# Performance work log

Hardware: AMD Instinct MI355X
Metric: run time of the kernel (lower is better)

Reference implementation:

```python
import jax, jax.numpy as jnp
import numpy as np

N_NODES, N_EDGES, N_FEAT, N_GRAPHS = 100_000, 1_600_000, 3, 512
FENG = jnp.array([4, 8, 9, 12, 13, 14])  # feng_filters(): second-order pairs with scale2 > scale1
LEAKY_SLOPE = 0.01


def _wavelet_constructor():
    # Psi_j = P^{2^{j-1}} - P^{2^j}, j = 1..4, over 17 diffusion levels P^0..P^16
    W = np.zeros((4, 17), dtype=np.float32)
    for j, (a, b) in enumerate([(1, 2), (2, 4), (4, 8), (8, 16)]):
        W[j, a] = 1.0
        W[j, b] = -1.0
    return jnp.asarray(W)


def _gcn_edges(edge_index, n):
    # gcn_norm with self-loops: w_ij = d_i^-1/2 d_j^-1/2 on A + I
    loop = jnp.arange(n)
    src = jnp.concatenate([edge_index[0], loop])
    dst = jnp.concatenate([edge_index[1], loop])
    deg = jax.ops.segment_sum(jnp.ones_like(dst, dtype=jnp.float32), dst, num_segments=n)
    dinv = jnp.where(deg > 0, jax.lax.rsqrt(deg), 0.0)
    w = dinv[src] * dinv[dst]
    return src, dst, w


def _diffuse(x, src, dst, w, n):
    # lazy random walk: 0.5 * (x + P_norm x), x: [N, C, k]
    agg = jax.ops.segment_sum(w[:, None, None] * x[src], dst, num_segments=n)
    return 0.5 * (x + agg)


def _scatter_features(x, edge_index):
    n, c = x.shape
    src, dst, w = _gcn_edges(edge_index, n)
    Wav = _wavelet_constructor()

    s0 = x[:, :, None]                                   # [N, C, 1]
    levels = [s0]
    for _ in range(16):
        levels.append(_diffuse(levels[-1], src, dst, w, n))
    D = jnp.stack(levels)                                # [17, N, C, 1]
    sub = jnp.einsum('wt,tnck->wnck', Wav, D)[..., 0]    # [4, N, C]
    s1 = jnp.abs(jnp.transpose(sub, (1, 2, 0)))          # [N, C, 4]

    levels2 = [s1]
    for _ in range(16):
        levels2.append(_diffuse(levels2[-1], src, dst, w, n))
    D2 = jnp.stack(levels2)                              # [17, N, C, 4]
    sub2 = jnp.einsum('wt,tncf->wncf', Wav, D2)          # [4, N, C, 4]
    # reproduce the exact torch transpose/reshape sequence of LEGS Scatter
    t = jnp.abs(jnp.transpose(sub2, (1, 0, 2, 3)).reshape(n, c, 16))  # [N, C, 16]
    s2 = jnp.swapaxes(t, 1, 2)[:, FENG]                  # [N, 6, C]

    xcat = jnp.concatenate([s0, s1], axis=2)             # [N, C, 5]
    xcat = jnp.swapaxes(xcat, 1, 2)                      # [N, 5, C]
    xcat = jnp.concatenate([xcat, s2], axis=1)           # [N, 11, C]
    return xcat.reshape(n, 11 * c)                       # [N, 33]


def _scatter_moments(x, batch, num_graphs):
    # per-graph mean / variance / skew (3 central moments), concatenated -> [G, 3*F]
    cnt = jax.ops.segment_sum(jnp.ones((x.shape[0],), x.dtype), batch, num_segments=num_graphs)
    cnt = jnp.maximum(cnt, 1.0)[:, None]
    mean = jax.ops.segment_sum(x, batch, num_segments=num_graphs) / cnt
    dev = x - mean[batch]
    var = jax.ops.segment_sum(dev * dev, batch, num_segments=num_graphs) / cnt
    skew = jax.ops.segment_sum(dev * dev * dev, batch, num_segments=num_graphs) / cnt
    return jnp.concatenate([mean, var, skew], axis=1)


def setup_inputs() -> dict:
    key = jax.random.key(0)
    ks = jax.random.split(key, 8)
    x = jax.random.normal(ks[0], (N_NODES, N_FEAT), dtype=jnp.float32)
    edge_index = jax.random.randint(ks[1], (2, N_EDGES), 0, N_NODES)
    batch = jnp.sort(jax.random.randint(ks[2], (N_NODES,), 0, N_GRAPHS))

    def lin(k, fan_in, fan_out):
        k1, k2 = jax.random.split(k)
        bound = 1.0 / np.sqrt(fan_in)
        W = jax.random.uniform(k1, (fan_in, fan_out), minval=-bound, maxval=bound, dtype=jnp.float32)
        b = jax.random.uniform(k2, (fan_out,), minval=-bound, maxval=bound, dtype=jnp.float32)
        return W, b

    W1, b1 = lin(ks[3], 99, 128)
    W2, b2 = lin(ks[4], 128, 64)
    W3, b3 = lin(ks[5], 64, 64)
    We, be = lin(ks[6], 64, 32)
    Wc, bc = lin(ks[7], 32, 1)
    return {"x": x, "W1": W1, "b1": b1, "W2": W2, "b2": b2, "W3": W3, "b3": b3,
            "We": We, "be": be, "Wc": Wc, "bc": bc,
            "edge_index": edge_index, "batch": batch, "num_graphs": N_GRAPHS}


def reference(x, W1, b1, W2, b2, W3, b3, We, be, Wc, bc, edge_index, batch, num_graphs):
    act = lambda v: jax.nn.leaky_relu(v, LEAKY_SLOPE)
    feats = _scatter_features(x, edge_index)              # [N, 33]
    h = _scatter_moments(feats, batch, num_graphs)        # [G, 99]
    h = act(h)
    h = act(h @ W1 + b1)        # dropout is identity (p=0.0)
    h = act(h @ W2 + b2)
    h = h @ W3 + b3             # no activation before embedding layer (as in source)
    embedding = h @ We + be
    output = embedding @ Wc + bc  # classifier applied to embedding (pre-activation)
    return embedding, output
```

## Files before the change

kernel.cpp:

```cpp
#include <hip/hip_runtime.h>

#define N_NODES 100000
#define N_EDGES 1600000
#define NG      512
#define NSB     98
#define SUBR    1024
#define SCAP    20480
#define SD      96
#define B2BLK   256
#define B2E     ((N_EDGES + B2BLK - 1) / B2BLK)
#define PCAP    18432

static __device__ __forceinline__ float lrelu(float v) {
    return v >= 0.0f ? v : 0.01f * v;
}

__global__ void k_zero_i32(int* __restrict__ p, int n) {
    int i = blockIdx.x * blockDim.x + threadIdx.x;
    if (i < n) p[i] = 0;
}

__global__ void k_dinv(const int* __restrict__ counts, float* __restrict__ dinv,
                       float* __restrict__ dinv2, float* __restrict__ sdeg) {
    int i = blockIdx.x * blockDim.x + threadIdx.x;
    if (i < N_NODES) {
        float deg = (float)(counts[i] + 1);
        float s = sqrtf(deg);
        sdeg[i] = s;
        dinv[i] = 1.0f / s;
        dinv2[i] = 1.0f / deg;
    }
}

__global__ __launch_bounds__(256) void k_bin2(const int* __restrict__ esrc,
                                              const int* __restrict__ edst,
                                              int* __restrict__ gcur,
                                              uint2* __restrict__ gbuf) {
    __shared__ uint2 st[NSB][SD];
    __shared__ int lcnt[NSB];
    __shared__ int gbase[NSB];
    for (int i = threadIdx.x; i < NSB; i += 256) lcnt[i] = 0;
    __syncthreads();
    int base = blockIdx.x * B2E;
    int end = base + B2E; if (end > N_EDGES) end = N_EDGES;
    for (int e = base + (int)threadIdx.x; e < end; e += 256) {
        int d = edst[e];
        int s = esrc[e];
        int b = d >> 10;
        int pos = atomicAdd(&lcnt[b], 1);
        if (pos < SD) {
            st[b][pos] = make_uint2((unsigned)s, (unsigned)d);
        } else {
            int g = atomicAdd(&gcur[b], 1);
            gbuf[(size_t)b * SCAP + g] = make_uint2((unsigned)s, (unsigned)d);
        }
    }
    __syncthreads();
    if (threadIdx.x < NSB) {
        int c = lcnt[threadIdx.x]; if (c > SD) c = SD;
        gbase[threadIdx.x] = atomicAdd(&gcur[threadIdx.x], c);
    }
    __syncthreads();
    for (int b = 0; b < NSB; ++b) {
        int cnt = lcnt[b]; if (cnt > SD) cnt = SD;
        int gb = gbase[b];
        for (int i = threadIdx.x; i < cnt; i += 256)
            gbuf[(size_t)b * SCAP + gb + i] = st[b][i];
    }
}

__global__ __launch_bounds__(256) void k_count_s(const int* __restrict__ gcur,
                                                 const uint2* __restrict__ gbuf,
                                                 int* __restrict__ counts) {
    __shared__ int h[SUBR];
    int sb = blockIdx.x;
    int lo = sb * SUBR;
    int nr = N_NODES - lo; if (nr > SUBR) nr = SUBR;
    for (int i = threadIdx.x; i < nr; i += 256) h[i] = 0;
    __syncthreads();
    int n = gcur[sb];
    const uint2* bb = gbuf + (size_t)sb * SCAP;
    for (int i = threadIdx.x; i < n; i += 256)
        atomicAdd(&h[(int)bb[i].y - lo], 1);
    __syncthreads();
    for (int i = threadIdx.x; i < nr; i += 256)
        counts[lo + i] = h[i];
}

__global__ void k_scan_block(const int* __restrict__ counts, int* __restrict__ offsets,
                             int* __restrict__ bsums, int n) {
    __shared__ int tmp[1024];
    int gid = blockIdx.x * 1024 + threadIdx.x;
    int v = (gid < n) ? counts[gid] : 0;
    tmp[threadIdx.x] = v;
    __syncthreads();
    for (int off = 1; off < 1024; off <<= 1) {
        int t = (threadIdx.x >= off) ? tmp[threadIdx.x - off] : 0;
        __syncthreads();
        tmp[threadIdx.x] += t;
        __syncthreads();
    }
    if (gid < n) offsets[gid + 1] = tmp[threadIdx.x];
    if (threadIdx.x == 1023) bsums[blockIdx.x] = tmp[1023];
}

__global__ void k_scan_bsums(int* __restrict__ bsums, int nb) {
    if (blockIdx.x == 0 && threadIdx.x == 0) {
        int acc = 0;
        for (int b = 0; b < nb; ++b) { int v = bsums[b]; bsums[b] = acc; acc += v; }
    }
}

__global__ void k_scan_add(int* __restrict__ offsets, const int* __restrict__ bsums, int n) {
    int gid = blockIdx.x * 1024 + threadIdx.x;
    if (gid < n) offsets[gid + 1] += bsums[blockIdx.x];
    if (gid == 0) offsets[0] = 0;
}

__global__ __launch_bounds__(256) void k_place(const int* __restrict__ gcur,
                                               const uint2* __restrict__ gbuf,
                                               const int* __restrict__ offsets,
                                               int* __restrict__ csr_src) {
    __shared__ int cur[SUBR];
    __shared__ int stage[PCAP];
    int sb = blockIdx.x;
    int lo = sb * SUBR;
    int nr = N_NODES - lo; if (nr > SUBR) nr = SUBR;
    int base = offsets[lo];
    int total = offsets[lo + nr] - base;
    for (int i = threadIdx.x; i < nr; i += 256)
        cur[i] = offsets[lo + i] - base;
    __syncthreads();
    int n = gcur[sb];
    const uint2* bb = gbuf + (size_t)sb * SCAP;
    for (int i = threadIdx.x; i < n; i += 256) {
        uint2 e = bb[i];
        int p = atomicAdd(&cur[(int)e.y - lo], 1);
        if (p < PCAP) stage[p] = (int)e.x;
        else csr_src[base + p] = (int)e.x;
    }
    __syncthreads();
    int wtot = total < PCAP ? total : PCAP;
    for (int i = threadIdx.x; i < wtot; i += 256)
        csr_src[base + i] = stage[i];
}

__global__ void k_vinit(const float* __restrict__ x, const float* __restrict__ dinv,
                        float4* __restrict__ v) {
    int i = blockIdx.x * blockDim.x + threadIdx.x;
    if (i >= N_NODES) return;
    float di = dinv[i];
    v[i] = make_float4(di * x[i * 3 + 0], di * x[i * 3 + 1], di * x[i * 3 + 2], 0.0f);
}

__global__ __launch_bounds__(256) void k_vdiff3(
    const float4* __restrict__ xin, float4* __restrict__ xout,
    const int* __restrict__ offs, const int* __restrict__ csrc,
    const float* __restrict__ dinv2) {
    int t = blockIdx.x * 256 + threadIdx.x;
    if (t >= N_NODES * 8) return;
    int h = t & 7;
    int i = t >> 3;
    int b = offs[i], e = offs[i + 1];
    float a0 = 0.0f, a1 = 0.0f, a2 = 0.0f;
    int p = b + h;
    while (p < e) {
        int idx[4];
        int c = 0;
#pragma unroll
        for (int j = 0; j < 4; ++j) {
            int pp = p + j * 8;
            if (pp < e) { idx[j] = csrc[pp]; c = j + 1; }
        }
#pragma unroll
        for (int j = 0; j < 4; ++j) {
            if (j < c) {
                float4 xv = xin[idx[j]];
                a0 += xv.x; a1 += xv.y; a2 += xv.z;
            }
        }
        p += 32;
    }
    a0 += __shfl_xor(a0, 1, 64); a1 += __shfl_xor(a1, 1, 64); a2 += __shfl_xor(a2, 1, 64);
    a0 += __shfl_xor(a0, 2, 64); a1 += __shfl_xor(a1, 2, 64); a2 += __shfl_xor(a2, 2, 64);
    a0 += __shfl_xor(a0, 4, 64); a1 += __shfl_xor(a1, 4, 64); a2 += __shfl_xor(a2, 4, 64);
    if (h == 0) {
        float d2 = dinv2[i];
        float4 sv = xin[i];
        xout[i] = make_float4(0.5f * (sv.x + d2 * (a0 + sv.x)),
                              0.5f * (sv.y + d2 * (a1 + sv.y)),
                              0.5f * (sv.z + d2 * (a2 + sv.z)), 0.0f);
    }
}

__global__ __launch_bounds__(256) void k_vdiff12(
    const float4* __restrict__ xin, float4* __restrict__ xout,
    const int* __restrict__ offs, const int* __restrict__ csrc,
    const float* __restrict__ dinv2) {
    int t = blockIdx.x * 256 + threadIdx.x;
    if (t >= N_NODES * 8) return;
    int h = t & 7;
    int i = t >> 3;
    int b = offs[i], e = offs[i + 1];
    float a[12];
#pragma unroll
    for (int c = 0; c < 12; ++c) a[c] = 0.0f;
    int p = b + h;
    while (p < e) {
        int idx[4];
        int c = 0;
#pragma unroll
        for (int j = 0; j < 4; ++j) {
            int pp = p + j * 8;
            if (pp < e) { idx[j] = csrc[pp]; c = j + 1; }
        }
#pragma unroll
        for (int j = 0; j < 4; ++j) {
            if (j < c) {
                int s = idx[j];
                float4 b0 = xin[s * 4 + 0];
                float4 b1 = xin[s * 4 + 1];
                float4 b2 = xin[s * 4 + 2];
                a[0] += b0.x; a[1] += b0.y; a[2]  += b0.z; a[3]  += b0.w;
                a[4] += b1.x; a[5] += b1.y; a[6]  += b1.z; a[7]  += b1.w;
                a[8] += b2.x; a[9] += b2.y; a[10] += b2.z; a[11] += b2.w;
            }
        }
        p += 32;
    }
#pragma unroll
    for (int c = 0; c < 12; ++c) {
        a[c] += __shfl_xor(a[c], 1, 64);
        a[c] += __shfl_xor(a[c], 2, 64);
        a[c] += __shfl_xor(a[c], 4, 64);
    }
    if (h == 0) {
        float d2 = dinv2[i];
        float4 s0 = xin[i * 4 + 0], s1 = xin[i * 4 + 1], s2 = xin[i * 4 + 2];
        xout[i * 4 + 0] = make_float4(0.5f * (s0.x + d2 * (a[0] + s0.x)),
                                      0.5f * (s0.y + d2 * (a[1] + s0.y)),
                                      0.5f * (s0.z + d2 * (a[2] + s0.z)),
                                      0.5f * (s0.w + d2 * (a[3] + s0.w)));
        xout[i * 4 + 1] = make_float4(0.5f * (s1.x + d2 * (a[4] + s1.x)),
                                      0.5f * (s1.y + d2 * (a[5] + s1.y)),
                                      0.5f * (s1.z + d2 * (a[6] + s1.z)),
                                      0.5f * (s1.w + d2 * (a[7] + s1.w)));
        xout[i * 4 + 2] = make_float4(0.5f * (s2.x + d2 * (a[8] + s2.x)),
                                      0.5f * (s2.y + d2 * (a[9] + s2.y)),
                                      0.5f * (s2.z + d2 * (a[10] + s2.z)),
                                      0.5f * (s2.w + d2 * (a[11] + s2.w)));
    }
}

__global__ void k_s1v(const float4* __restrict__ L1, const float4* __restrict__ L2,
                      const float4* __restrict__ L4, const float4* __restrict__ L8,
                      const float4* __restrict__ L16, float* __restrict__ s1vp) {
    int i = blockIdx.x * blockDim.x + threadIdx.x;
    if (i >= N_NODES) return;
    float4 v[5];
    v[0] = L1[i]; v[1] = L2[i]; v[2] = L4[i]; v[3] = L8[i]; v[4] = L16[i];
    float* out = s1vp + (size_t)i * 16;
#pragma unroll
    for (int f = 0; f < 4; ++f) {
        out[0 * 4 + f] = fabsf(v[f].x - v[f + 1].x);
        out[1 * 4 + f] = fabsf(v[f].y - v[f + 1].y);
        out[2 * 4 + f] = fabsf(v[f].z - v[f + 1].z);
    }
}

__global__ void k_feats(const float* __restrict__ x, const float* __restrict__ s1vp,
                        const float* __restrict__ M1, const float* __restrict__ M2,
                        const float* __restrict__ M4, const float* __restrict__ M8,
                        const float* __restrict__ M16, const float* __restrict__ sdeg,
                        float* __restrict__ feats) {
    int i = blockIdx.x * blockDim.x + threadIdx.x;
    if (i >= N_NODES) return;
    float sd = sdeg[i];
    float* out = feats + (size_t)i * 33;
    out[0] = x[i * 3 + 0];
    out[1] = x[i * 3 + 1];
    out[2] = x[i * 3 + 2];
    for (int r = 1; r <= 4; ++r)
        for (int c = 0; c < 3; ++c)
            out[r * 3 + c] = sd * s1vp[(size_t)i * 16 + c * 4 + (r - 1)];
    const float* Ms[5] = {M1, M2, M4, M8, M16};
    const int FENG[6] = {4, 8, 9, 12, 13, 14};
    for (int m = 0; m < 6; ++m) {
        for (int c2 = 0; c2 < 3; ++c2) {
            int idx = c2 * 16 + FENG[m];
            int w = idx / 12, rem = idx % 12, cc = rem / 4, f = rem % 4;
            float v = Ms[w][(size_t)i * 16 + cc * 4 + f] - Ms[w + 1][(size_t)i * 16 + cc * 4 + f];
            out[(5 + m) * 3 + c2] = fabsf(sd * v);
        }
    }
}

static __device__ __forceinline__ int lower_bound_i(const int* __restrict__ a, int n, int key) {
    int lo = 0, hi = n;
    while (lo < hi) { int mid = (lo + hi) >> 1; if (a[mid] < key) lo = mid + 1; else hi = mid; }
    return lo;
}

__global__ __launch_bounds__(256) void k_moments(
    const float* __restrict__ feats, const int* __restrict__ batch,
    float* __restrict__ h0) {
    __shared__ float P1[4][33], P2[4][33], P3[4][33];
    int g = blockIdx.x;
    int lo = lower_bound_i(batch, N_NODES, g);
    int hi = lower_bound_i(batch, N_NODES, g + 1);
    int w = threadIdx.x >> 6;
    int l = threadIdx.x & 63;
    float s1 = 0.0f, s2 = 0.0f, s3 = 0.0f;
    if (l < 33) {
        for (int i = lo + w; i < hi; i += 4) {
            float v = feats[(size_t)i * 33 + l];
            s1 += v;
            s2 += v * v;
            s3 += v * v * v;
        }
        P1[w][l] = s1; P2[w][l] = s2; P3[w][l] = s3;
    }
    __syncthreads();
    if (threadIdx.x < 33) {
        int c = threadIdx.x;
        float S1 = P1[0][c] + P1[1][c] + P1[2][c] + P1[3][c];
        float S2 = P2[0][c] + P2[1][c] + P2[2][c] + P2[3][c];
        float S3 = P3[0][c] + P3[1][c] + P3[2][c] + P3[3][c];
        float cnt = (float)((hi - lo) > 1 ? (hi - lo) : 1);
        float mu  = S1 / cnt;
        float ex2 = S2 / cnt;
        float ex3 = S3 / cnt;
        float var = ex2 - mu * mu;
        float skw = ex3 - 3.0f * mu * ex2 + 2.0f * mu * mu * mu;
        h0[g * 99 + c]      = lrelu(mu);
        h0[g * 99 + 33 + c] = lrelu(var);
        h0[g * 99 + 66 + c] = lrelu(skw);
    }
}

__global__ __launch_bounds__(128) void k_mlp(
    const float* __restrict__ h0,
    const float* __restrict__ W1, const float* __restrict__ b1,
    const float* __restrict__ W2, const float* __restrict__ b2,
    const float* __restrict__ W3, const float* __restrict__ b3,
    const float* __restrict__ We, const float* __restrict__ be,
    const float* __restrict__ Wc, const float* __restrict__ bc,
    float* __restrict__ emb, float* __restrict__ outp) {
    __shared__ float s0[99], s1[128], s2[64], s3[64], s4[32];
    int g = blockIdx.x;
    int t = threadIdx.x;
    if (t < 99) s0[t] = h0[g * 99 + t];
    __syncthreads();
    {
        float a = b1[t];
        for (int k = 0; k < 99; ++k) a += s0[k] * W1[k * 128 + t];
        s1[t] = lrelu(a);
    }
    __syncthreads();
    if (t < 64) {
        float a = b2[t];
        for (int k = 0; k < 128; ++k) a += s1[k] * W2[k * 64 + t];
        s2[t] = lrelu(a);
    }
    __syncthreads();
    if (t < 64) {
        float a = b3[t];
        for (int k = 0; k < 64; ++k) a += s2[k] * W3[k * 64 + t];
        s3[t] = a;
    }
    __syncthreads();
    if (t < 32) {
        float a = be[t];
        for (int k = 0; k < 64; ++k) a += s3[k] * We[k * 32 + t];
        s4[t] = a;
        emb[g * 32 + t] = a;
    }
    __syncthreads();
    if (t == 0) {
        float a = bc[0];
        for (int k = 0; k < 32; ++k) a += s4[k] * Wc[k];
        outp[g] = a;
    }
}

extern "C" void kernel_launch(void* const* d_in, const int* in_sizes, int n_in,
                              void* d_out, int out_size, void* d_ws, size_t ws_size,
                              hipStream_t stream) {
    const float* x   = (const float*)d_in[0];
    const float* W1  = (const float*)d_in[1];
    const float* b1  = (const float*)d_in[2];
    const float* W2  = (const float*)d_in[3];
    const float* b2  = (const float*)d_in[4];
    const float* W3  = (const float*)d_in[5];
    const float* b3  = (const float*)d_in[6];
    const float* We  = (const float*)d_in[7];
    const float* be  = (const float*)d_in[8];
    const float* Wc  = (const float*)d_in[9];
    const float* bc  = (const float*)d_in[10];
    const int*   eix = (const int*)d_in[11];
    const int*   batch = (const int*)d_in[12];
    const int* esrc = eix;
    const int* edst = eix + N_EDGES;

    char* ws = (char*)d_ws;
    size_t off = 0;
    auto alloc = [&](size_t bytes) -> void* {
        void* p = ws + off;
        off = (off + bytes + 255) & ~(size_t)255;
        return p;
    };
    int*   counts  = (int*)alloc((size_t)N_NODES * 4);
    int*   offsets = (int*)alloc((size_t)(N_NODES + 1) * 4);
    float* dinv    = (float*)alloc((size_t)N_NODES * 4);
    float* dinv2   = (float*)alloc((size_t)N_NODES * 4);
    float* sdeg    = (float*)alloc((size_t)N_NODES * 4);
    int*   bsums   = (int*)alloc(1024 * 4);
    int*   gcur    = (int*)alloc(NSB * 4);
    uint2* gbuf    = (uint2*)alloc((size_t)NSB * SCAP * 8);
    int*   csr_src = (int*)alloc((size_t)N_EDGES * 4);
    float4* v0     = (float4*)alloc((size_t)N_NODES * 16);
    float4* p1[7];
    for (int i = 0; i < 7; ++i) p1[i] = (float4*)alloc((size_t)N_NODES * 16);
    float* s1vp = (float*)alloc((size_t)N_NODES * 16 * 4);
    float* p2[7];
    for (int i = 0; i < 7; ++i) p2[i] = (float*)alloc((size_t)N_NODES * 16 * 4);
    float* feats = (float*)alloc((size_t)N_NODES * 33 * 4);
    float* h0 = (float*)alloc((size_t)NG * 99 * 4);
    (void)ws_size; (void)in_sizes; (void)n_in; (void)out_size;

    const int TB = 256;
    const int gbN = (N_NODES + TB - 1) / TB;
    const int nbScan = (N_NODES + 1023) / 1024;

    hipLaunchKernelGGL(k_zero_i32, dim3(1), dim3(TB), 0, stream, gcur, NSB);
    hipLaunchKernelGGL(k_bin2, dim3(B2BLK), dim3(TB), 0, stream, esrc, edst, gcur, gbuf);
    hipLaunchKernelGGL(k_count_s, dim3(NSB), dim3(TB), 0, stream, gcur, gbuf, counts);
    hipLaunchKernelGGL(k_dinv, dim3(gbN), dim3(TB), 0, stream, counts, dinv, dinv2, sdeg);
    hipLaunchKernelGGL(k_scan_block, dim3(nbScan), dim3(1024), 0, stream, counts, offsets, bsums, N_NODES);
    hipLaunchKernelGGL(k_scan_bsums, dim3(1), dim3(1), 0, stream, bsums, nbScan);
    hipLaunchKernelGGL(k_scan_add, dim3(nbScan), dim3(1024), 0, stream, offsets, bsums, N_NODES);
    hipLaunchKernelGGL(k_place, dim3(NSB), dim3(TB), 0, stream, gcur, gbuf, offsets, csr_src);

    hipLaunchKernelGGL(k_vinit, dim3(gbN), dim3(TB), 0, stream, x, dinv, v0);

    const int saveT[5] = {1, 2, 4, 8, 16};

    const float4* prev = v0;
    float4* saves1[5];
    {
        int si = 0, sc = 0;
        const int gb = (N_NODES * 8 + TB - 1) / TB;
        for (int t = 1; t <= 16; ++t) {
            float4* outb;
            if (si < 5 && t == saveT[si]) { outb = p1[si]; saves1[si] = outb; ++si; }
            else { outb = p1[5 + sc]; sc ^= 1; }
            hipLaunchKernelGGL(k_vdiff3, dim3(gb), dim3(TB), 0, stream,
                               prev, outb, offsets, csr_src, dinv2);
            prev = outb;
        }
    }
    hipLaunchKernelGGL(k_s1v, dim3(gbN), dim3(TB), 0, stream,
                       saves1[0], saves1[1], saves1[2], saves1[3], saves1[4], s1vp);

    float* saves2[5];
    {
        const float* prev2 = s1vp;
        int si = 0, sc = 0;
        const int gb = (N_NODES * 8 + TB - 1) / TB;
        for (int t = 1; t <= 16; ++t) {
            float* outb;
            if (si < 5 && t == saveT[si]) { outb = p2[si]; saves2[si] = outb; ++si; }
            else { outb = p2[5 + sc]; sc ^= 1; }
            hipLaunchKernelGGL(k_vdiff12, dim3(gb), dim3(TB), 0, stream,
                               (const float4*)prev2, (float4*)outb, offsets, csr_src, dinv2);
            prev2 = outb;
        }
    }

    hipLaunchKernelGGL(k_feats, dim3(gbN), dim3(TB), 0, stream,
                       x, s1vp, saves2[0], saves2[1], saves2[2], saves2[3], saves2[4], sdeg, feats);
    hipLaunchKernelGGL(k_moments, dim3(NG), dim3(256), 0, stream, feats, batch, h0);

    float* emb  = (float*)d_out;
    float* outp = (float*)d_out + NG * 32;
    hipLaunchKernelGGL(k_mlp, dim3(NG), dim3(128), 0, stream,
                       h0, W1, b1, W2, b2, W3, b3, We, be, Wc, bc, emb, outp);
}
```

Baseline: 716.6 us.

## Fuse preprocessing, epilogues and head kernels to cut launch count

Merges the degree-inverse and vinit kernels, replaces the three-kernel global scan with a per-superblock scan inside k_place plus a tiny superblock-base scan, and folds the s1 wavelet computation and feature assembly into the last diffusion step of each stage via a LAST template. The moments and MLP kernels become one head kernel. The aim is to drop about seven launches and the round trips through intermediate buffers such as the level-16 outputs and h0. In exchange, the last diffusion kernels run heavier epilogues on one thread per node, which adds register pressure.

```diff
diff --git a/kernel.cpp b/kernel.cpp
--- a/kernel.cpp
+++ b/kernel.cpp
@@ -20,15 +20,17 @@
     if (i < n) p[i] = 0;
 }
 
-__global__ void k_dinv(const int* __restrict__ counts, float* __restrict__ dinv,
-                       float* __restrict__ dinv2, float* __restrict__ sdeg) {
+__global__ void k_dinv_vinit(const int* __restrict__ counts, const float* __restrict__ x,
+                             float* __restrict__ dinv2, float* __restrict__ sdeg,
+                             float4* __restrict__ v0) {
     int i = blockIdx.x * blockDim.x + threadIdx.x;
     if (i < N_NODES) {
         float deg = (float)(counts[i] + 1);
         float s = sqrtf(deg);
         sdeg[i] = s;
-        dinv[i] = 1.0f / s;
         dinv2[i] = 1.0f / deg;
+        float di = 1.0f / s;
+        v0[i] = make_float4(di * x[i * 3 + 0], di * x[i * 3 + 1], di * x[i * 3 + 2], 0.0f);
     }
 }
 
@@ -87,76 +89,77 @@
         counts[lo + i] = h[i];
 }
 
-__global__ void k_scan_block(const int* __restrict__ counts, int* __restrict__ offsets,
-                             int* __restrict__ bsums, int n) {
-    __shared__ int tmp[1024];
-    int gid = blockIdx.x * 1024 + threadIdx.x;
-    int v = (gid < n) ? counts[gid] : 0;
-    tmp[threadIdx.x] = v;
-    __syncthreads();
-    for (int off = 1; off < 1024; off <<= 1) {
-        int t = (threadIdx.x >= off) ? tmp[threadIdx.x - off] : 0;
-        __syncthreads();
-        tmp[threadIdx.x] += t;
-        __syncthreads();
-    }
-    if (gid < n) offsets[gid + 1] = tmp[threadIdx.x];
-    if (threadIdx.x == 1023) bsums[blockIdx.x] = tmp[1023];
-}
-
-__global__ void k_scan_bsums(int* __restrict__ bsums, int nb) {
+__global__ void k_sbscan(const int* __restrict__ gcur, int* __restrict__ sbbase) {
     if (blockIdx.x == 0 && threadIdx.x == 0) {
         int acc = 0;
-        for (int b = 0; b < nb; ++b) { int v = bsums[b]; bsums[b] = acc; acc += v; }
-    }
-}
-
-__global__ void k_scan_add(int* __restrict__ offsets, const int* __restrict__ bsums, int n) {
-    int gid = blockIdx.x * 1024 + threadIdx.x;
-    if (gid < n) offsets[gid + 1] += bsums[blockIdx.x];
-    if (gid == 0) offsets[0] = 0;
+        for (int b = 0; b < NSB; ++b) { sbbase[b] = acc; acc += gcur[b]; }
+    }
 }
 
 __global__ __launch_bounds__(256) void k_place(const int* __restrict__ gcur,
                                                const uint2* __restrict__ gbuf,
-                                               const int* __restrict__ offsets,
+                                               const int* __restrict__ sbbase,
+                                               const int* __restrict__ counts,
+                                               int* __restrict__ offsets,
                                                int* __restrict__ csr_src) {
     __shared__ int cur[SUBR];
+    __shared__ int wsum[256];
     __shared__ int stage[PCAP];
     int sb = blockIdx.x;
     int lo = sb * SUBR;
     int nr = N_NODES - lo; if (nr > SUBR) nr = SUBR;
-    int base = offsets[lo];
-    int total = offsets[lo + nr] - base;
-    for (int i = threadIdx.x; i < nr; i += 256)
-        cur[i] = offsets[lo + i] - base;
+    int t = threadIdx.x;
+    int c0[4];
+    int b4 = t * 4;
+    int s = 0;
+#pragma unroll
+    for (int j = 0; j < 4; ++j) {
+        int ii = b4 + j;
+        c0[j] = (ii < nr) ? counts[lo + ii] : 0;
+        s += c0[j];
+    }
+    wsum[t] = s;
+    __syncthreads();
+    for (int off = 1; off < 256; off <<= 1) {
+        int v = (t >= off) ? wsum[t - off] : 0;
+        __syncthreads();
+        wsum[t] += v;
+        __syncthreads();
+    }
+    int run = (t == 0) ? 0 : wsum[t - 1];
+#pragma unroll
+    for (int j = 0; j < 4; ++j) {
+        int ii = b4 + j;
+        if (ii < SUBR) cur[ii] = run;
+        run += c0[j];
+    }
+    __syncthreads();
+    int gb = sbbase[sb];
+    for (int i = t; i < nr; i += 256) offsets[lo + i] = gb + cur[i];
+    if (sb == NSB - 1 && t == 0) offsets[N_NODES] = N_EDGES;
     __syncthreads();
     int n = gcur[sb];
     const uint2* bb = gbuf + (size_t)sb * SCAP;
-    for (int i = threadIdx.x; i < n; i += 256) {
+    for (int i = t; i < n; i += 256) {
         uint2 e = bb[i];
         int p = atomicAdd(&cur[(int)e.y - lo], 1);
         if (p < PCAP) stage[p] = (int)e.x;
-        else csr_src[base + p] = (int)e.x;
-    }
-    __syncthreads();
-    int wtot = total < PCAP ? total : PCAP;
-    for (int i = threadIdx.x; i < wtot; i += 256)
-        csr_src[base + i] = stage[i];
-}
-
-__global__ void k_vinit(const float* __restrict__ x, const float* __restrict__ dinv,
-                        float4* __restrict__ v) {
-    int i = blockIdx.x * blockDim.x + threadIdx.x;
-    if (i >= N_NODES) return;
-    float di = dinv[i];
-    v[i] = make_float4(di * x[i * 3 + 0], di * x[i * 3 + 1], di * x[i * 3 + 2], 0.0f);
-}
-
+        else csr_src[gb + p] = (int)e.x;
+    }
+    __syncthreads();
+    int wtot = n < PCAP ? n : PCAP;
+    for (int i = t; i < wtot; i += 256)
+        csr_src[gb + i] = stage[i];
+}
+
+template <bool LAST>
 __global__ __launch_bounds__(256) void k_vdiff3(
     const float4* __restrict__ xin, float4* __restrict__ xout,
     const int* __restrict__ offs, const int* __restrict__ csrc,
-    const float* __restrict__ dinv2) {
+    const float* __restrict__ dinv2,
+    const float4* __restrict__ L1, const float4* __restrict__ L2,
+    const float4* __restrict__ L4, const float4* __restrict__ L8,
+    float* __restrict__ s1vp) {
     int t = blockIdx.x * 256 + threadIdx.x;
     if (t >= N_NODES * 8) return;
     int h = t & 7;
@@ -187,16 +190,39 @@
     if (h == 0) {
         float d2 = dinv2[i];
         float4 sv = xin[i];
-        xout[i] = make_float4(0.5f * (sv.x + d2 * (a0 + sv.x)),
-                              0.5f * (sv.y + d2 * (a1 + sv.y)),
-                              0.5f * (sv.z + d2 * (a2 + sv.z)), 0.0f);
-    }
-}
-
+        float o0 = 0.5f * (sv.x + d2 * (a0 + sv.x));
+        float o1 = 0.5f * (sv.y + d2 * (a1 + sv.y));
+        float o2 = 0.5f * (sv.z + d2 * (a2 + sv.z));
+        if (!LAST) {
+            xout[i] = make_float4(o0, o1, o2, 0.0f);
+        } else {
+            float4 l0 = L1[i], l1 = L2[i], l2 = L4[i], l3 = L8[i];
+            float* out = s1vp + (size_t)i * 16;
+            out[0]  = fabsf(l0.x - l1.x);
+            out[1]  = fabsf(l1.x - l2.x);
+            out[2]  = fabsf(l2.x - l3.x);
+            out[3]  = fabsf(l3.x - o0);
+            out[4]  = fabsf(l0.y - l1.y);
+            out[5]  = fabsf(l1.y - l2.y);
+            out[6]  = fabsf(l2.y - l3.y);
+            out[7]  = fabsf(l3.y - o1);
+            out[8]  = fabsf(l0.z - l1.z);
+            out[9]  = fabsf(l1.z - l2.z);
+            out[10] = fabsf(l2.z - l3.z);
+            out[11] = fabsf(l3.z - o2);
+        }
+    }
+}
+
+template <bool LAST>
 __global__ __launch_bounds__(256) void k_vdiff12(
     const float4* __restrict__ xin, float4* __restrict__ xout,
     const int* __restrict__ offs, const int* __restrict__ csrc,
-    const float* __restrict__ dinv2) {
+    const float* __restrict__ dinv2,
+    const float* __restrict__ M1, const float* __restrict__ M2,
+    const float* __restrict__ M4, const float* __restrict__ M8,
+    const float* __restrict__ x, const float* __restrict__ sdeg,
+    const float* __restrict__ s1vp, float* __restrict__ feats) {
     int t = blockIdx.x * 256 + threadIdx.x;
     if (t >= N_NODES * 8) return;
     int h = t & 7;
@@ -237,60 +263,39 @@
     if (h == 0) {
         float d2 = dinv2[i];
         float4 s0 = xin[i * 4 + 0], s1 = xin[i * 4 + 1], s2 = xin[i * 4 + 2];
-        xout[i * 4 + 0] = make_float4(0.5f * (s0.x + d2 * (a[0] + s0.x)),
-                                      0.5f * (s0.y + d2 * (a[1] + s0.y)),
-                                      0.5f * (s0.z + d2 * (a[2] + s0.z)),
-                                      0.5f * (s0.w + d2 * (a[3] + s0.w)));
-        xout[i * 4 + 1] = make_float4(0.5f * (s1.x + d2 * (a[4] + s1.x)),
-                                      0.5f * (s1.y + d2 * (a[5] + s1.y)),
-                                      0.5f * (s1.z + d2 * (a[6] + s1.z)),
-                                      0.5f * (s1.w + d2 * (a[7] + s1.w)));
-        xout[i * 4 + 2] = make_float4(0.5f * (s2.x + d2 * (a[8] + s2.x)),
-                                      0.5f * (s2.y + d2 * (a[9] + s2.y)),
-                                      0.5f * (s2.z + d2 * (a[10] + s2.z)),
-                                      0.5f * (s2.w + d2 * (a[11] + s2.w)));
-    }
-}
-
-__global__ void k_s1v(const float4* __restrict__ L1, const float4* __restrict__ L2,
-                      const float4* __restrict__ L4, const float4* __restrict__ L8,
-                      const float4* __restrict__ L16, float* __restrict__ s1vp) {
-    int i = blockIdx.x * blockDim.x + threadIdx.x;
-    if (i >= N_NODES) return;
-    float4 v[5];
-    v[0] = L1[i]; v[1] = L2[i]; v[2] = L4[i]; v[3] = L8[i]; v[4] = L16[i];
-    float* out = s1vp + (size_t)i * 16;
-#pragma unroll
-    for (int f = 0; f < 4; ++f) {
-        out[0 * 4 + f] = fabsf(v[f].x - v[f + 1].x);
-        out[1 * 4 + f] = fabsf(v[f].y - v[f + 1].y);
-        out[2 * 4 + f] = fabsf(v[f].z - v[f + 1].z);
-    }
-}
-
-__global__ void k_feats(const float* __restrict__ x, const float* __restrict__ s1vp,
-                        const float* __restrict__ M1, const float* __restrict__ M2,
-                        const float* __restrict__ M4, const float* __restrict__ M8,
-                        const float* __restrict__ M16, const float* __restrict__ sdeg,
-                        float* __restrict__ feats) {
-    int i = blockIdx.x * blockDim.x + threadIdx.x;
-    if (i >= N_NODES) return;
-    float sd = sdeg[i];
-    float* out = feats + (size_t)i * 33;
-    out[0] = x[i * 3 + 0];
-    out[1] = x[i * 3 + 1];
-    out[2] = x[i * 3 + 2];
-    for (int r = 1; r <= 4; ++r)
-        for (int c = 0; c < 3; ++c)
-            out[r * 3 + c] = sd * s1vp[(size_t)i * 16 + c * 4 + (r - 1)];
-    const float* Ms[5] = {M1, M2, M4, M8, M16};
-    const int FENG[6] = {4, 8, 9, 12, 13, 14};
-    for (int m = 0; m < 6; ++m) {
-        for (int c2 = 0; c2 < 3; ++c2) {
-            int idx = c2 * 16 + FENG[m];
-            int w = idx / 12, rem = idx % 12, cc = rem / 4, f = rem % 4;
-            float v = Ms[w][(size_t)i * 16 + cc * 4 + f] - Ms[w + 1][(size_t)i * 16 + cc * 4 + f];
-            out[(5 + m) * 3 + c2] = fabsf(sd * v);
+        float sv[12] = {s0.x, s0.y, s0.z, s0.w, s1.x, s1.y, s1.z, s1.w,
+                        s2.x, s2.y, s2.z, s2.w};
+        float o[12];
+#pragma unroll
+        for (int c = 0; c < 12; ++c) o[c] = 0.5f * (sv[c] + d2 * (a[c] + sv[c]));
+        if (!LAST) {
+            xout[i * 4 + 0] = make_float4(o[0], o[1], o[2], o[3]);
+            xout[i * 4 + 1] = make_float4(o[4], o[5], o[6], o[7]);
+            xout[i * 4 + 2] = make_float4(o[8], o[9], o[10], o[11]);
+        } else {
+            float sd = sdeg[i];
+            float* out = feats + (size_t)i * 33;
+            out[0] = x[i * 3 + 0];
+            out[1] = x[i * 3 + 1];
+            out[2] = x[i * 3 + 2];
+#pragma unroll
+            for (int r = 1; r <= 4; ++r)
+#pragma unroll
+                for (int c = 0; c < 3; ++c)
+                    out[r * 3 + c] = sd * s1vp[(size_t)i * 16 + c * 4 + (r - 1)];
+            const float* Ms[4] = {M1, M2, M4, M8};
+            const int FENG[6] = {4, 8, 9, 12, 13, 14};
+#pragma unroll
+            for (int m = 0; m < 6; ++m) {
+#pragma unroll
+                for (int c2 = 0; c2 < 3; ++c2) {
+                    int idx = c2 * 16 + FENG[m];
+                    int w = idx / 12, rem = idx % 12, cc = rem / 4, f = rem % 4;
+                    float va = (w < 4)     ? Ms[w][(size_t)i * 16 + cc * 4 + f]     : o[rem];
+                    float vb = (w + 1 < 4) ? Ms[w + 1][(size_t)i * 16 + cc * 4 + f] : o[rem];
+                    out[(5 + m) * 3 + c2] = fabsf(sd * (va - vb));
+                }
+            }
         }
     }
 }
@@ -301,10 +306,17 @@
     return lo;
 }
 
-__global__ __launch_bounds__(256) void k_moments(
+__global__ __launch_bounds__(256) void k_head(
     const float* __restrict__ feats, const int* __restrict__ batch,
-    float* __restrict__ h0) {
+    const float* __restrict__ W1, const float* __restrict__ b1,
+    const float* __restrict__ W2, const float* __restrict__ b2,
+    const float* __restrict__ W3, const float* __restrict__ b3,
+    const float* __restrict__ We, const float* __restrict__ be,
+    const float* __restrict__ Wc, const float* __restrict__ bc,
+    float* __restrict__ emb, float* __restrict__ outp) {
     __shared__ float P1[4][33], P2[4][33], P3[4][33];
+    __shared__ float h0s[99];
+    __shared__ float y1[128], y2[64], y3[64], y4[32];
     int g = blockIdx.x;
     int lo = lower_bound_i(batch, N_NODES, g);
     int hi = lower_bound_i(batch, N_NODES, g + 1);
@@ -332,54 +344,41 @@
         float ex3 = S3 / cnt;
         float var = ex2 - mu * mu;
         float skw = ex3 - 3.0f * mu * ex2 + 2.0f * mu * mu * mu;
-        h0[g * 99 + c]      = lrelu(mu);
-        h0[g * 99 + 33 + c] = lrelu(var);
-        h0[g * 99 + 66 + c] = lrelu(skw);
-    }
-}
-
-__global__ __launch_bounds__(128) void k_mlp(
-    const float* __restrict__ h0,
-    const float* __restrict__ W1, const float* __restrict__ b1,
-    const float* __restrict__ W2, const float* __restrict__ b2,
-    const float* __restrict__ W3, const float* __restrict__ b3,
-    const float* __restrict__ We, const float* __restrict__ be,
-    const float* __restrict__ Wc, const float* __restrict__ bc,
-    float* __restrict__ emb, float* __restrict__ outp) {
-    __shared__ float s0[99], s1[128], s2[64], s3[64], s4[32];
-    int g = blockIdx.x;
+        h0s[c]      = lrelu(mu);
+        h0s[33 + c] = lrelu(var);
+        h0s[66 + c] = lrelu(skw);
+    }
+    __syncthreads();
     int t = threadIdx.x;
-    if (t < 99) s0[t] = h0[g * 99 + t];
-    __syncthreads();
-    {
-        float a = b1[t];
-        for (int k = 0; k < 99; ++k) a += s0[k] * W1[k * 128 + t];
-        s1[t] = lrelu(a);
+    if (t < 128) {
+        float acc = b1[t];
+        for (int k = 0; k < 99; ++k) acc += h0s[k] * W1[k * 128 + t];
+        y1[t] = lrelu(acc);
     }
     __syncthreads();
     if (t < 64) {
-        float a = b2[t];
-        for (int k = 0; k < 128; ++k) a += s1[k] * W2[k * 64 + t];
-        s2[t] = lrelu(a);
+        float acc = b2[t];
+        for (int k = 0; k < 128; ++k) acc += y1[k] * W2[k * 64 + t];
+        y2[t] = lrelu(acc);
     }
     __syncthreads();
     if (t < 64) {
-        float a = b3[t];
-        for (int k = 0; k < 64; ++k) a += s2[k] * W3[k * 64 + t];
-        s3[t] = a;
+        float acc = b3[t];
+        for (int k = 0; k < 64; ++k) acc += y2[k] * W3[k * 64 + t];
+        y3[t] = acc;
     }
     __syncthreads();
     if (t < 32) {
-        float a = be[t];
-        for (int k = 0; k < 64; ++k) a += s3[k] * We[k * 32 + t];
-        s4[t] = a;
-        emb[g * 32 + t] = a;
+        float acc = be[t];
+        for (int k = 0; k < 64; ++k) acc += y3[k] * We[k * 32 + t];
+        y4[t] = acc;
+        emb[g * 32 + t] = acc;
     }
     __syncthreads();
     if (t == 0) {
-        float a = bc[0];
-        for (int k = 0; k < 32; ++k) a += s4[k] * Wc[k];
-        outp[g] = a;
+        float acc = bc[0];
+        for (int k = 0; k < 32; ++k) acc += y4[k] * Wc[k];
+        outp[g] = acc;
     }
 }
 
@@ -411,11 +410,10 @@
     };
     int*   counts  = (int*)alloc((size_t)N_NODES * 4);
     int*   offsets = (int*)alloc((size_t)(N_NODES + 1) * 4);
-    float* dinv    = (float*)alloc((size_t)N_NODES * 4);
     float* dinv2   = (float*)alloc((size_t)N_NODES * 4);
     float* sdeg    = (float*)alloc((size_t)N_NODES * 4);
-    int*   bsums   = (int*)alloc(1024 * 4);
     int*   gcur    = (int*)alloc(NSB * 4);
+    int*   sbbase  = (int*)alloc(NSB * 4);
     uint2* gbuf    = (uint2*)alloc((size_t)NSB * SCAP * 8);
     int*   csr_src = (int*)alloc((size_t)N_EDGES * 4);
     float4* v0     = (float4*)alloc((size_t)N_NODES * 16);
@@ -425,23 +423,18 @@
     float* p2[7];
     for (int i = 0; i < 7; ++i) p2[i] = (float*)alloc((size_t)N_NODES * 16 * 4);
     float* feats = (float*)alloc((size_t)N_NODES * 33 * 4);
-    float* h0 = (float*)alloc((size_t)NG * 99 * 4);
     (void)ws_size; (void)in_sizes; (void)n_in; (void)out_size;
 
     const int TB = 256;
     const int gbN = (N_NODES + TB - 1) / TB;
-    const int nbScan = (N_NODES + 1023) / 1024;
 
     hipLaunchKernelGGL(k_zero_i32, dim3(1), dim3(TB), 0, stream, gcur, NSB);
     hipLaunchKernelGGL(k_bin2, dim3(B2BLK), dim3(TB), 0, stream, esrc, edst, gcur, gbuf);
     hipLaunchKernelGGL(k_count_s, dim3(NSB), dim3(TB), 0, stream, gcur, gbuf, counts);
-    hipLaunchKernelGGL(k_dinv, dim3(gbN), dim3(TB), 0, stream, counts, dinv, dinv2, sdeg);
-    hipLaunchKernelGGL(k_scan_block, dim3(nbScan), dim3(1024), 0, stream, counts, offsets, bsums, N_NODES);
-    hipLaunchKernelGGL(k_scan_bsums, dim3(1), dim3(1), 0, stream, bsums, nbScan);
-    hipLaunchKernelGGL(k_scan_add, dim3(nbScan), dim3(1024), 0, stream, offsets, bsums, N_NODES);
-    hipLaunchKernelGGL(k_place, dim3(NSB), dim3(TB), 0, stream, gcur, gbuf, offsets, csr_src);
-
-    hipLaunchKernelGGL(k_vinit, dim3(gbN), dim3(TB), 0, stream, x, dinv, v0);
+    hipLaunchKernelGGL(k_dinv_vinit, dim3(gbN), dim3(TB), 0, stream, counts, x, dinv2, sdeg, v0);
+    hipLaunchKernelGGL(k_sbscan, dim3(1), dim3(64), 0, stream, gcur, sbbase);
+    hipLaunchKernelGGL(k_place, dim3(NSB), dim3(TB), 0, stream,
+                       gcur, gbuf, sbbase, counts, offsets, csr_src);
 
     const int saveT[5] = {1, 2, 4, 8, 16};
 
@@ -454,13 +447,20 @@
             float4* outb;
             if (si < 5 && t == saveT[si]) { outb = p1[si]; saves1[si] = outb; ++si; }
             else { outb = p1[5 + sc]; sc ^= 1; }
-            hipLaunchKernelGGL(k_vdiff3, dim3(gb), dim3(TB), 0, stream,
-                               prev, outb, offsets, csr_src, dinv2);
+            if (t < 16) {
+                hipLaunchKernelGGL((k_vdiff3<false>), dim3(gb), dim3(TB), 0, stream,
+                                   prev, outb, offsets, csr_src, dinv2,
+                                   (const float4*)nullptr, (const float4*)nullptr,
+                                   (const float4*)nullptr, (const float4*)nullptr,
+                                   (float*)nullptr);
+            } else {
+                hipLaunchKernelGGL((k_vdiff3<true>), dim3(gb), dim3(TB), 0, stream,
+                                   prev, outb, offsets, csr_src, dinv2,
+                                   saves1[0], saves1[1], saves1[2], saves1[3], s1vp);
+            }
             prev = outb;
         }
     }
-    hipLaunchKernelGGL(k_s1v, dim3(gbN), dim3(TB), 0, stream,
-                       saves1[0], saves1[1], saves1[2], saves1[3], saves1[4], s1vp);
 
     float* saves2[5];
     {
@@ -471,18 +471,25 @@
             float* outb;
             if (si < 5 && t == saveT[si]) { outb = p2[si]; saves2[si] = outb; ++si; }
             else { outb = p2[5 + sc]; sc ^= 1; }
-            hipLaunchKernelGGL(k_vdiff12, dim3(gb), dim3(TB), 0, stream,
-                               (const float4*)prev2, (float4*)outb, offsets, csr_src, dinv2);
+            if (t < 16) {
+                hipLaunchKernelGGL((k_vdiff12<false>), dim3(gb), dim3(TB), 0, stream,
+                                   (const float4*)prev2, (float4*)outb, offsets, csr_src, dinv2,
+                                   (const float*)nullptr, (const float*)nullptr,
+                                   (const float*)nullptr, (const float*)nullptr,
+                                   (const float*)nullptr, (const float*)nullptr,
+                                   (const float*)nullptr, (float*)nullptr);
+            } else {
+                hipLaunchKernelGGL((k_vdiff12<true>), dim3(gb), dim3(TB), 0, stream,
+                                   (const float4*)prev2, (float4*)outb, offsets, csr_src, dinv2,
+                                   saves2[0], saves2[1], saves2[2], saves2[3],
+                                   x, sdeg, s1vp, feats);
+            }
             prev2 = outb;
         }
     }
-
-    hipLaunchKernelGGL(k_feats, dim3(gbN), dim3(TB), 0, stream,
-                       x, s1vp, saves2[0], saves2[1], saves2[2], saves2[3], saves2[4], sdeg, feats);
-    hipLaunchKernelGGL(k_moments, dim3(NG), dim3(256), 0, stream, feats, batch, h0);
 
     float* emb  = (float*)d_out;
     float* outp = (float*)d_out + NG * 32;
-    hipLaunchKernelGGL(k_mlp, dim3(NG), dim3(128), 0, stream,
-                       h0, W1, b1, W2, b2, W3, b3, We, be, Wc, bc, emb, outp);
-}
+    hipLaunchKernelGGL(k_head, dim3(NG), dim3(TB), 0, stream,
+                       feats, batch, W1, b1, W2, b2, W3, b3, We, be, Wc, bc, emb, outp);
+}
```

Measured after the change: 687.6 us. 1.04x faster.
